# Kernel optimization log

Measured on AMD Instinct MI355X. Metric: run time of the kernel, lower is better.

The kernel has to match this reference:

```python
import jax, jax.numpy as jnp
import numpy as np

K, M_EMB, N_HID, D_CTX, D_ATT, M_COV = 128, 256, 256, 684, 512, 256
B, H, W = 64, 16, 48


def gru_cell(x, h, W_ih, W_hh, b_ih, b_hh):
    # PyTorch GRUCell semantics
    gi = x @ W_ih.T + b_ih
    gh = h @ W_hh.T + b_hh
    i_r, i_z, i_n = jnp.split(gi, 3, axis=-1)
    h_r, h_z, h_n = jnp.split(gh, 3, axis=-1)
    r = jax.nn.sigmoid(i_r + h_r)
    z = jax.nn.sigmoid(i_z + h_z)
    n = jnp.tanh(i_n + r * h_n)
    return (1.0 - z) * n + z * h


def setup_inputs() -> dict:
    key = jax.random.key(0)
    ks = jax.random.split(key, 24)
    s = 0.02
    inp = {
        'y': jax.random.randint(ks[0], (B,), 0, K),
        'y_mask': jnp.ones((B,), jnp.float32),
        'context': jax.random.normal(ks[1], (B, D_CTX, H, W), jnp.float32),
        'pre_hidden': jax.random.normal(ks[2], (B, N_HID), jnp.float32),
        'alpha_past': jax.random.uniform(ks[3], (B, H, W), jnp.float32),
        'emb': jax.random.normal(ks[4], (K + 1, M_EMB)) * s,
        'W_ih1': jax.random.normal(ks[5], (3 * N_HID, M_EMB)) * s,
        'W_hh1': jax.random.normal(ks[6], (3 * N_HID, N_HID)) * s,
        'b_ih1': jnp.zeros((3 * N_HID,)),
        'b_hh1': jnp.zeros((3 * N_HID,)),
        'conv_Ua_w': jax.random.normal(ks[7], (D_ATT, D_CTX, 1, 1)) * s,
        'conv_Ua_b': jnp.zeros((D_ATT,)),
        'Wa': jax.random.normal(ks[8], (D_ATT, N_HID)) * s,
        'conv_Q_w': jax.random.normal(ks[9], (M_COV, 1, 3, 3)) * s,
        'Uf': jax.random.normal(ks[10], (D_ATT, M_COV)) * s,
        'Uf_b': jnp.zeros((D_ATT,)),
        'va': jax.random.normal(ks[11], (1, D_ATT)) * s,
        'va_b': jnp.zeros((1,)),
        'W_ih2': jax.random.normal(ks[12], (3 * N_HID, D_CTX)) * s,
        'W_hh2': jax.random.normal(ks[13], (3 * N_HID, N_HID)) * s,
        'b_ih2': jnp.zeros((3 * N_HID,)),
        'b_hh2': jnp.zeros((3 * N_HID,)),
        'Wct': jax.random.normal(ks[14], (M_EMB, D_CTX)) * s,
        'Wct_b': jnp.zeros((M_EMB,)),
        'Wht': jax.random.normal(ks[15], (M_EMB, N_HID)) * s,
        'Wht_b': jnp.zeros((M_EMB,)),
        'W0': jax.random.normal(ks[16], (K, M_EMB // 2)) * s,
        'W0_b': jnp.zeros((K,)),
    }
    return inp


def reference(y, y_mask, context, pre_hidden, alpha_past, emb,
              W_ih1, W_hh1, b_ih1, b_hh1, conv_Ua_w, conv_Ua_b, Wa,
              conv_Q_w, Uf, Uf_b, va, va_b,
              W_ih2, W_hh2, b_ih2, b_hh2, Wct, Wct_b, Wht, Wht_b, W0, W0_b):
    embedded = emb[y]                                           # [B, m]
    s_hat = gru_cell(embedded, pre_hidden, W_ih1, W_hh1, b_ih1, b_hh1)
    s_hat = y_mask[:, None] * s_hat + (1.0 - y_mask)[:, None] * pre_hidden

    Wa_h1 = s_hat @ Wa.T                                        # [B, A]
    # 1x1 conv == channel projection, output in NHWC layout
    Ua_ctx = jnp.einsum('bdhw,ad->bhwa', context, conv_Ua_w[:, :, 0, 0]) + conv_Ua_b
    # 3x3 coverage conv over past attention map
    cover_F = jax.lax.conv_general_dilated(
        alpha_past[:, None, :, :], conv_Q_w, (1, 1), 'SAME',
        dimension_numbers=('NCHW', 'OIHW', 'NCHW'))              # [B, M, H, W]
    cover_F = jnp.transpose(cover_F, (0, 2, 3, 1))               # [B, H, W, M]
    cover_vector = cover_F @ Uf.T + Uf_b                         # [B, H, W, A]

    e_att = jnp.tanh(Ua_ctx + Wa_h1[:, None, None, :] + cover_vector)
    alpha = (e_att @ va.T + va_b)[..., 0].reshape(e_att.shape[0], -1)  # [B, H*W]
    alpha = jax.nn.softmax(alpha, axis=1)

    ct = jnp.einsum('bdp,bp->bd', context.reshape(context.shape[0], context.shape[1], -1), alpha)

    s = gru_cell(ct, s_hat, W_ih2, W_hh2, b_ih2, b_hh2)
    s = y_mask[:, None] * s + (1.0 - y_mask)[:, None] * s_hat

    logit = ct @ Wct.T + Wct_b + s @ Wht.T + Wht_b + embedded    # [B, m]
    logit = logit.reshape(logit.shape[0], -1, 2).max(axis=2)     # maxout -> [B, m/2]
    out = logit @ W0.T + W0_b                                    # [B, K]
    return out, s, alpha.reshape(alpha.shape[0], H, W)
```

## Files before the change

### kernel.cpp

```cpp
#include <hip/hip_runtime.h>
#include <hip/hip_bf16.h>
#include <math.h>

#define BB 64
#define KV 128
#define ME 256
#define NH 256
#define DC 684
#define DA 512
#define MC 256
#define HH_ 16
#define WW_ 48
#define HW_ 768
#define NS 22

typedef __attribute__((ext_vector_type(8))) short bf16x8;
typedef __attribute__((ext_vector_type(4))) float f32x4;

#define WS_G     0
#define WS_RB    (WS_G + 4608)
#define WS_EMB   (WS_RB + 32768)
#define WS_SH    (WS_EMB + 16384)
#define WS_AL    (WS_SH + 16384)
#define WS_CT    (WS_AL + 49152)
#define WS_APACK (WS_CT + 43776)
#define WS_GI    (WS_APACK + 180224)
#define WS_GH    (WS_GI + 49152)
#define WS_LG    WS_GI
#define WS_BP    (WS_GH + 49152)
#define NEED_BYTES ((size_t)441600 * 4 + (size_t)34603008 * 2)

static __device__ __forceinline__ unsigned short f2b(float v) {
    __hip_bfloat16 h = __float2bfloat16(v);
    return *reinterpret_cast<unsigned short*>(&h);
}

static __device__ __forceinline__ void gl_lds16(const unsigned short* g,
                                                unsigned short* l) {
    __builtin_amdgcn_global_load_lds(
        (const __attribute__((address_space(1))) unsigned int*)g,
        (__attribute__((address_space(3))) unsigned int*)l, 16, 0, 0);
}

__global__ __launch_bounds__(512) void k_prep(
    const float* __restrict__ ctx, const float* __restrict__ Ua,
    const float* __restrict__ Uf, const float* __restrict__ convQ,
    const int* __restrict__ y, const float* __restrict__ emb,
    unsigned short* __restrict__ Bpack, unsigned short* __restrict__ Apack,
    float* __restrict__ G, float* __restrict__ embedded) {
    __shared__ unsigned short Ts[64 * 360];
    int bx = blockIdx.x, t = threadIdx.x;
    if (bx < 768) {
        int b = bx / 12, pt = bx % 12, p0 = pt * 64;
        int w = t >> 6, p = t & 63;
        unsigned short* dst = Bpack + (long)(b * 12 + pt) * 22 * 2048;
        for (int ch = 0; ch < 2; ch++) {
            int dbase = ch * 352;
            if (ch) __syncthreads();
#pragma unroll
            for (int iter = 0; iter < 11; iter++) {
                int d0 = dbase + iter * 32 + w * 4;
                float v0 = 0.f, v1 = 0.f, v2 = 0.f, v3 = 0.f;
                const float* src = ctx + ((long)b * DC + d0) * HW_ + p0 + p;
                if (d0 + 0 < DC) v0 = src[0];
                if (d0 + 1 < DC) v1 = src[HW_];
                if (d0 + 2 < DC) v2 = src[2 * HW_];
                if (d0 + 3 < DC) v3 = src[3 * HW_];
                unsigned u01 = (unsigned)f2b(v0) | ((unsigned)f2b(v1) << 16);
                unsigned u23 = (unsigned)f2b(v2) | ((unsigned)f2b(v3) << 16);
                *(uint2*)&Ts[p * 360 + (d0 - dbase)] = make_uint2(u01, u23);
            }
            __syncthreads();
            int so = t >> 8;
            int tt = t & 255;
            int pp = tt >> 2, slot = tt & 3;
#pragma unroll
            for (int s2 = 0; s2 < 12; s2 += 2) {
                int sl = s2 + so;
                if (sl < 11) {
                    int s = ch * 11 + sl;
                    bf16x8 v = *(const bf16x8*)&Ts[pp * 360 + sl * 32 +
                                                   ((slot ^ ((pp >> 1) & 3))
                                                    << 3)];
                    *(bf16x8*)(dst + (long)(s * 256 + tt) * 8) = v;
                }
            }
        }
    } else if (bx < 856) {
        int bi = bx - 768;
#pragma unroll
        for (int r = 0; r < 8; r++) {
            int idx = bi * 4096 + r * 512 + t;
            int e = idx & 7, slot = (idx >> 3) & 3;
            int a = (idx >> 5) & 511, s = idx >> 14;
            int d = s * 32 + ((slot ^ ((a >> 1) & 3)) << 3) + e;
            float v = (d < DC) ? Ua[a * DC + d] : 0.f;
            Apack[idx] = f2b(v);
        }
    } else if (bx < 865) {
        int idx = (bx - 856) * 512 + t;
        if (idx < DA * 9) {
            int a = idx / 9, k = idx % 9;
            float s = 0.f;
            for (int m = 0; m < MC; m++) s += Uf[a * MC + m] * convQ[m * 9 + k];
            G[idx] = s;
        }
    } else {
        int b = bx - 865;
        if (t < ME) embedded[b * ME + t] = emb[y[b] * ME + t];
    }
}

__global__ __launch_bounds__(256) void k_G(const float* __restrict__ Uf,
                                           const float* __restrict__ convQ,
                                           float* __restrict__ G) {
    int idx = blockIdx.x * 256 + threadIdx.x;
    if (idx >= DA * 9) return;
    int a = idx / 9, k = idx % 9;
    float s = 0.f;
    for (int m = 0; m < MC; m++) s += Uf[a * MC + m] * convQ[m * 9 + k];
    G[idx] = s;
}

__global__ __launch_bounds__(256) void k_prepA(const float* __restrict__ Ua,
                                               unsigned short* __restrict__ Apack) {
    int idx = blockIdx.x * 256 + threadIdx.x;
    if (idx >= NS * DA * 32) return;
    int e = idx & 7, slot = (idx >> 3) & 3;
    int a = (idx >> 5) & 511, s = idx >> 14;
    int d = s * 32 + ((slot ^ ((a >> 1) & 3)) << 3) + e;
    float v = (d < DC) ? Ua[a * DC + d] : 0.f;
    Apack[idx] = f2b(v);
}

__global__ __launch_bounds__(256) void k_emb(const int* __restrict__ y,
                                             const float* __restrict__ emb,
                                             float* __restrict__ embedded) {
    int b = blockIdx.x, t = threadIdx.x;
    embedded[b * ME + t] = emb[y[b] * ME + t];
}

__global__ __launch_bounds__(256) void k_rows256(
    const float* __restrict__ X, const float* __restrict__ W,
    const float* __restrict__ bias, const float* __restrict__ bias2,
    float* __restrict__ out, int outStride) {
    __shared__ float Xs[64 * 257];
    __shared__ float Ws[4 * 260];
    int t = threadIdx.x, w = t >> 6, lane = t & 63;
    for (int i = t; i < 64 * 256; i += 256) {
        int bb = i >> 8, k = i & 255;
        Xs[bb * 257 + k] = X[bb * 256 + k];
    }
    int r = blockIdx.x * 4 + w;
    *(f32x4*)(Ws + w * 260 + lane * 4) = *(const f32x4*)(W + r * 256 + lane * 4);
    __syncthreads();
    const float* xrow = Xs + lane * 257;
    const float* wrow = Ws + w * 260;
    float acc = 0.f;
#pragma unroll 8
    for (int k = 0; k < 256; k++) acc += wrow[k] * xrow[k];
    acc += bias[r];
    if (bias2) acc += bias2[r];
    out[lane * outStride + r] = acc;
}

__global__ __launch_bounds__(256) void k_gih1(
    const float* __restrict__ embedded, const float* __restrict__ pre_hidden,
    const float* __restrict__ W_ih1, const float* __restrict__ W_hh1,
    const float* __restrict__ b_ih1, const float* __restrict__ b_hh1,
    float* __restrict__ gi, float* __restrict__ gh) {
    __shared__ float Xs[64 * 257];
    __shared__ float Ws[4 * 260];
    int bx = blockIdx.x, t = threadIdx.x, w = t >> 6, lane = t & 63;
    const float *X, *W, *bias;
    float* outp;
    int r;
    if (bx < 192) {
        X = embedded; W = W_ih1; bias = b_ih1; outp = gi; r = bx * 4 + w;
    } else {
        X = pre_hidden; W = W_hh1; bias = b_hh1; outp = gh; r = (bx - 192) * 4 + w;
    }
    for (int i = t; i < 64 * 256; i += 256) {
        int bb = i >> 8, k = i & 255;
        Xs[bb * 257 + k] = X[bb * 256 + k];
    }
    *(f32x4*)(Ws + w * 260 + lane * 4) = *(const f32x4*)(W + r * 256 + lane * 4);
    __syncthreads();
    const float* xrow = Xs + lane * 257;
    const float* wrow = Ws + w * 260;
    float acc = 0.f;
#pragma unroll 8
    for (int k = 0; k < 256; k++) acc += wrow[k] * xrow[k];
    outp[lane * 768 + r] = acc + bias[r];
}

__global__ __launch_bounds__(256) void k_gih2(
    const float* __restrict__ ctv, const float* __restrict__ s_hat,
    const float* __restrict__ W_ih2, const float* __restrict__ W_hh2,
    const float* __restrict__ b_ih2, const float* __restrict__ b_hh2,
    float* __restrict__ gi, float* __restrict__ gh) {
    __shared__ float Xs[64 * 257];
    __shared__ float Ws[4 * 260];
    int bx = blockIdx.x, t = threadIdx.x, w = t >> 6, lane = t & 63;
    if (bx < 192) {
        int r = bx * 4 + w;
        float acc = 0.f;
        for (int c = 0; c < 3; c++) {
            int c0 = c * 228;
            __syncthreads();
            for (int i = t; i < 64 * 228; i += 256) {
                int bb = i / 228, kk = i - bb * 228;
                Xs[bb * 229 + kk] = ctv[bb * DC + c0 + kk];
            }
            for (int j = lane; j < 228; j += 64)
                Ws[w * 260 + j] = W_ih2[r * DC + c0 + j];
            __syncthreads();
            const float* xrow = Xs + lane * 229;
            const float* wrow = Ws + w * 260;
#pragma unroll 4
            for (int k = 0; k < 228; k++) acc += wrow[k] * xrow[k];
        }
        gi[lane * 768 + r] = acc + b_ih2[r];
    } else {
        int r = (bx - 192) * 4 + w;
        for (int i = t; i < 64 * 256; i += 256) {
            int bb = i >> 8, k = i & 255;
            Xs[bb * 257 + k] = s_hat[bb * 256 + k];
        }
        *(f32x4*)(Ws + w * 260 + lane * 4) =
            *(const f32x4*)(W_hh2 + r * 256 + lane * 4);
        __syncthreads();
        const float* xrow = Xs + lane * 257;
        const float* wrow = Ws + w * 260;
        float acc = 0.f;
#pragma unroll 8
        for (int k = 0; k < 256; k++) acc += wrow[k] * xrow[k];
        gh[lane * 768 + r] = acc + b_hh2[r];
    }
}

__global__ __launch_bounds__(256) void k_gru(const float* __restrict__ gi,
                                             const float* __restrict__ gh,
                                             const float* __restrict__ h,
                                             const float* __restrict__ y_mask,
                                             float* __restrict__ outp) {
    int b = blockIdx.x, t = threadIdx.x;
    float hv = h[b * NH + t];
    float r = 1.f / (1.f + expf(-(gi[b * 768 + t] + gh[b * 768 + t])));
    float z = 1.f / (1.f + expf(-(gi[b * 768 + 256 + t] + gh[b * 768 + 256 + t])));
    float n = tanhf(gi[b * 768 + 512 + t] + r * gh[b * 768 + 512 + t]);
    float sv = (1.f - z) * n + z * hv;
    float m = y_mask[b];
    outp[b * NH + t] = m * sv + (1.f - m) * hv;
}

__global__ __launch_bounds__(512) void k_att_cnt(
    const unsigned short* __restrict__ Apack,
    const unsigned short* __restrict__ Bpack, const float* __restrict__ G,
    const float* __restrict__ rb, const float* __restrict__ va,
    const float* __restrict__ va_b, const float* __restrict__ apast,
    float* __restrict__ alogit) {
    __shared__ __attribute__((aligned(16))) unsigned short lsA[2][16384];
    __shared__ __attribute__((aligned(16))) unsigned short lsB[2][2048];
    __shared__ float ap_s[18 * 50];
    __shared__ float part_s[8][64];
    int pt = blockIdx.x, b = blockIdx.y;
    int t = threadIdx.x, w = t >> 6, lane = t & 63;
    int l15 = lane & 15, lg = lane >> 4;
    int sx = lg ^ ((l15 >> 1) & 3);

    for (int idx = t; idx < 900; idx += 512) {
        int hh = idx / 50, ww = idx % 50;
        float v = 0.f;
        if (hh >= 1 && hh <= HH_ && ww >= 1 && ww <= WW_)
            v = apast[b * HW_ + (hh - 1) * WW_ + (ww - 1)];
        ap_s[idx] = v;
    }
    __syncthreads();

    const unsigned short* Asrc = Apack + w * 2048 + lane * 8;
    const unsigned short* Bsrc =
        Bpack + (long)(b * 12 + pt) * 22 * 2048 + (w & 3) * 512 + lane * 8;

#define STAGE(S, BUF)                                                        \
    do {                                                                     \
        _Pragma("unroll") for (int i_ = 0; i_ < 4; i_++)                     \
            gl_lds16(Asrc + (long)(S)*16384 + i_ * 512,                      \
                     &lsA[BUF][w * 2048 + i_ * 512]);                        \
        gl_lds16(Bsrc + (long)(S)*2048, &lsB[BUF][(w & 3) * 512]);           \
    } while (0)

#define STEP_BODY(CUR)                                                       \
    do {                                                                     \
        bf16x8 af[4], bf[4];                                                 \
        _Pragma("unroll") for (int j = 0; j < 4; j++)                        \
            bf[j] = *(const bf16x8*)&lsB[CUR][(j * 16 + l15) * 32 + sx * 8]; \
        _Pragma("unroll") for (int i = 0; i < 4; i++)                        \
            af[i] = *(const bf16x8*)&lsA[CUR][(w * 64 + i * 16 + l15) * 32 + \
                                             sx * 8];                        \
        _Pragma("unroll") for (int i = 0; i < 4; i++)                        \
            _Pragma("unroll") for (int j = 0; j < 4; j++)                    \
                acc[i][j] = __builtin_amdgcn_mfma_f32_16x16x32_bf16(         \
                    af[i], bf[j], acc[i][j], 0, 0, 0);                       \
    } while (0)

    f32x4 acc[4][4];
#pragma unroll
    for (int i = 0; i < 4; i++)
#pragma unroll
        for (int j = 0; j < 4; j++) acc[i][j] = {0.f, 0.f, 0.f, 0.f};

    STAGE(0, 0);
    STAGE(1, 1);

    for (int s = 0; s < NS - 1; s++) {
        int cur = s & 1;
        asm volatile("s_waitcnt vmcnt(5)" ::: "memory");
        __builtin_amdgcn_sched_barrier(0);
        __builtin_amdgcn_s_barrier();
        __builtin_amdgcn_sched_barrier(0);
        STEP_BODY(cur);
        __builtin_amdgcn_s_barrier();
        __builtin_amdgcn_sched_barrier(0);
        if (s + 2 < NS) STAGE(s + 2, cur);
    }
    asm volatile("s_waitcnt vmcnt(0)" ::: "memory");
    __builtin_amdgcn_sched_barrier(0);
    __builtin_amdgcn_s_barrier();
    __builtin_amdgcn_sched_barrier(0);
    STEP_BODY((NS - 1) & 1);
#undef STAGE
#undef STEP_BODY

    float partial[4] = {0.f, 0.f, 0.f, 0.f};
#pragma unroll
    for (int i = 0; i < 4; i++) {
#pragma unroll
        for (int r = 0; r < 4; r++) {
            int a = w * 64 + i * 16 + lg * 4 + r;
            float rbv = rb[b * DA + a];
            float vav = va[a];
            const float* Ga = G + a * 9;
            float g0 = Ga[0], g1 = Ga[1], g2 = Ga[2], g3 = Ga[3], g4 = Ga[4];
            float g5 = Ga[5], g6 = Ga[6], g7 = Ga[7], g8 = Ga[8];
#pragma unroll
            for (int j = 0; j < 4; j++) {
                int p = pt * 64 + j * 16 + l15;
                int hh = p / WW_, ww = p % WW_;
                const float* ap = ap_s + hh * 50 + ww;
                float cov = g0 * ap[0] + g1 * ap[1] + g2 * ap[2] +
                            g3 * ap[50] + g4 * ap[51] + g5 * ap[52] +
                            g6 * ap[100] + g7 * ap[101] + g8 * ap[102];
                float e = tanhf(acc[i][j][r] + rbv + cov);
                partial[j] += vav * e;
            }
        }
    }
#pragma unroll
    for (int j = 0; j < 4; j++) {
        partial[j] += __shfl_xor(partial[j], 16);
        partial[j] += __shfl_xor(partial[j], 32);
    }
    if (lane < 16) {
#pragma unroll
        for (int j = 0; j < 4; j++) part_s[w][j * 16 + lane] = partial[j];
    }
    __syncthreads();
    if (t < 64) {
        float sum = va_b[0];
#pragma unroll
        for (int q = 0; q < 8; q++) sum += part_s[q][t];
        alogit[b * HW_ + pt * 64 + t] = sum;
    }
}

#define LDW 40
__global__ __launch_bounds__(256) void k_att_lds(
    const unsigned short* __restrict__ Apack, const float* __restrict__ ctx,
    const float* __restrict__ G, const float* __restrict__ rb,
    const float* __restrict__ va, const float* __restrict__ va_b,
    const float* __restrict__ apast, float* __restrict__ alogit) {
    __shared__ __attribute__((aligned(16))) short lsB[2][64 * LDW];
    __shared__ float ap_s[18 * 50];
    __shared__ float part_s[4 * 64];
    int b = blockIdx.y;
    int p0 = blockIdx.x * 64;
    int t = threadIdx.x;
    int w = t >> 6, lane = t & 63;
    int l15 = lane & 15, lg = lane >> 4;
    int sxA = lg ^ ((l15 >> 1) & 3);
    int pq = t & 15, kp = t >> 4;
    const float* ctx_b = ctx + (long)b * DC * HW_ + p0;

    for (int idx = t; idx < 900; idx += 256) {
        int hh = idx / 50, ww = idx % 50;
        float v = 0.f;
        if (hh >= 1 && hh <= HH_ && ww >= 1 && ww <= WW_)
            v = apast[b * HW_ + (hh - 1) * WW_ + (ww - 1)];
        ap_s[idx] = v;
    }

#define CTXLOAD(FA, FB, S)                                                   \
    do {                                                                     \
        int d_ = (S) * 32 + 2 * kp;                                          \
        const float* s0_ = ctx_b + (long)d_ * HW_ + pq;                      \
        bool g0_ = d_ < DC, g1_ = (d_ + 1) < DC;                             \
        _Pragma("unroll") for (int j_ = 0; j_ < 4; j_++) {                   \
            FA[j_] = g0_ ? s0_[16 * j_] : 0.f;                               \
            FB[j_] = g1_ ? s0_[HW_ + 16 * j_] : 0.f;                         \
        }                                                                    \
    } while (0)
#define STAGEW(FA, FB, BUF)                                                  \
    do {                                                                     \
        _Pragma("unroll") for (int j_ = 0; j_ < 4; j_++) {                   \
            ((unsigned*)lsB[BUF])[(pq + 16 * j_) * (LDW / 2) + kp] =         \
                (unsigned)f2b(FA[j_]) | ((unsigned)f2b(FB[j_]) << 16);       \
        }                                                                    \
    } while (0)
#define ALOAD(AF, S)                                                         \
    do {                                                                     \
        _Pragma("unroll") for (int i_ = 0; i_ < 8; i_++)                     \
            AF[i_] = *(const bf16x8*)(Apack +                                \
                ((long)((S)*512 + w * 128 + i_ * 16 + l15) * 4 + sxA) * 8);  \
    } while (0)
#define BREAD(BF, BUF)                                                       \
    do {                                                                     \
        _Pragma("unroll") for (int j_ = 0; j_ < 4; j_++)                     \
            BF[j_] = *(const bf16x8*)(&lsB[BUF][(j_ * 16 + l15) * LDW +      \
                                               lg * 8]);                     \
    } while (0)
#define MFMA8x4(AF, BF)                                                      \
    do {                                                                     \
        _Pragma("unroll") for (int i_ = 0; i_ < 8; i_++)                     \
            _Pragma("unroll") for (int j_ = 0; j_ < 4; j_++)                 \
                acc[i_][j_] = __builtin_amdgcn_mfma_f32_16x16x32_bf16(       \
                    AF[i_], BF[j_], acc[i_][j_], 0, 0, 0);                   \
    } while (0)

    f32x4 acc[8][4];
#pragma unroll
    for (int i = 0; i < 8; i++)
#pragma unroll
        for (int j = 0; j < 4; j++) acc[i][j] = {0.f, 0.f, 0.f, 0.f};

    float fa0[4], fb0[4], fa1[4], fb1[4];
    bf16x8 afr0[8], afr1[8], bfr[4];

    CTXLOAD(fa1, fb1, 0);
    ALOAD(afr0, 0);
    STAGEW(fa1, fb1, 0);
    CTXLOAD(fa1, fb1, 1);
    __syncthreads();

    for (int ss = 0; ss < NS; ss += 2) {
        if (ss + 2 < NS) CTXLOAD(fa0, fb0, ss + 2);
        ALOAD(afr1, ss + 1);
        BREAD(bfr, 0);
        STAGEW(fa1, fb1, 1);
        MFMA8x4(afr0, bfr);
        __syncthreads();
        if (ss + 3 < NS) CTXLOAD(fa1, fb1, ss + 3);
        if (ss + 2 < NS) {
            ALOAD(afr0, ss + 2);
            BREAD(bfr, 1);
            STAGEW(fa0, fb0, 0);
            MFMA8x4(afr1, bfr);
        } else {
            BREAD(bfr, 1);
            MFMA8x4(afr1, bfr);
        }
        __syncthreads();
    }

    float partial[4] = {0.f, 0.f, 0.f, 0.f};
#pragma unroll
    for (int i = 0; i < 8; i++) {
#pragma unroll
        for (int r = 0; r < 4; r++) {
            int a = w * 128 + i * 16 + lg * 4 + r;
            float rbv = rb[b * DA + a];
            float vav = va[a];
            const float* Ga = G + a * 9;
            float g0 = Ga[0], g1 = Ga[1], g2 = Ga[2], g3 = Ga[3], g4 = Ga[4];
            float g5 = Ga[5], g6 = Ga[6], g7 = Ga[7], g8 = Ga[8];
#pragma unroll
            for (int j = 0; j < 4; j++) {
                int p = p0 + j * 16 + l15;
                int hh = p / WW_, ww = p % WW_;
                const float* ap = ap_s + hh * 50 + ww;
                float cov = g0 * ap[0] + g1 * ap[1] + g2 * ap[2] +
                            g3 * ap[50] + g4 * ap[51] + g5 * ap[52] +
                            g6 * ap[100] + g7 * ap[101] + g8 * ap[102];
                float e = tanhf(acc[i][j][r] + rbv + cov);
                partial[j] += vav * e;
            }
        }
    }
#pragma unroll
    for (int j = 0; j < 4; j++) {
        partial[j] += __shfl_xor(partial[j], 16);
        partial[j] += __shfl_xor(partial[j], 32);
    }
    if (lane < 16) {
#pragma unroll
        for (int j = 0; j < 4; j++) part_s[w * 64 + j * 16 + lane] = partial[j];
    }
    __syncthreads();
    if (t < 64) {
        float s = va_b[0] + part_s[t] + part_s[64 + t] + part_s[128 + t] +
                  part_s[192 + t];
        alogit[b * HW_ + p0 + t] = s;
    }
}

__global__ __launch_bounds__(256) void k_ctsm(const float* __restrict__ ctx,
                                              const float* __restrict__ alogit,
                                              float* __restrict__ ct,
                                              float* __restrict__ alpha_out) {
    __shared__ float al_s[HW_];
    __shared__ float red[16];
    int b = blockIdx.y, t = threadIdx.x;
    float v[3];
    float mx = -1e30f;
    for (int i = 0; i < 3; i++) {
        v[i] = alogit[b * HW_ + i * 256 + t];
        mx = fmaxf(mx, v[i]);
    }
    for (int off = 32; off > 0; off >>= 1) mx = fmaxf(mx, __shfl_down(mx, off));
    if ((t & 63) == 0) red[t >> 6] = mx;
    __syncthreads();
    if (t == 0) red[0] = fmaxf(fmaxf(red[0], red[1]), fmaxf(red[2], red[3]));
    __syncthreads();
    mx = red[0];
    float sum = 0.f;
    for (int i = 0; i < 3; i++) {
        v[i] = expf(v[i] - mx);
        sum += v[i];
    }
    for (int off = 32; off > 0; off >>= 1) sum += __shfl_down(sum, off);
    if ((t & 63) == 0) red[8 + (t >> 6)] = sum;
    __syncthreads();
    if (t == 0) red[8] = red[8] + red[9] + red[10] + red[11];
    __syncthreads();
    float inv = 1.f / red[8];
    for (int i = 0; i < 3; i++) {
        float a = v[i] * inv;
        al_s[i * 256 + t] = a;
        if (blockIdx.x == 0) alpha_out[b * HW_ + i * 256 + t] = a;
    }
    __syncthreads();
    int dc0 = blockIdx.x * 114;
    int wave = t >> 6, lane = t & 63;
    for (int d = dc0 + wave; d < dc0 + 114; d += 4) {
        const float* row = &ctx[((long)b * DC + d) * HW_];
        float s = 0.f;
#pragma unroll
        for (int q = 0; q < 12; q++) s += row[lane + q * 64] * al_s[lane + q * 64];
        for (int off = 32; off > 0; off >>= 1) s += __shfl_down(s, off);
        if (lane == 0) ct[b * DC + d] = s;
    }
}

__global__ __launch_bounds__(256) void k_logit(
    const float* __restrict__ ctv, const float* __restrict__ s,
    const float* __restrict__ embedded, const float* __restrict__ Wct,
    const float* __restrict__ Wht, const float* __restrict__ Wct_b,
    const float* __restrict__ Wht_b, float* __restrict__ lg) {
    __shared__ float Xs[64 * 257];
    __shared__ float Ws[4 * 232];
    int t = threadIdx.x, w = t >> 6, lane = t & 63;
    int r = blockIdx.x * 4 + w;
    float acc = 0.f;
    for (int c = 0; c < 3; c++) {
        int c0 = c * 228;
        __syncthreads();
        for (int i = t; i < 64 * 228; i += 256) {
            int bb = i / 228, kk = i - bb * 228;
            Xs[bb * 229 + kk] = ctv[bb * DC + c0 + kk];
        }
        for (int j = lane; j < 228; j += 64) Ws[w * 232 + j] = Wct[r * DC + c0 + j];
        __syncthreads();
        const float* xrow = Xs + lane * 229;
        const float* wrow = Ws + w * 232;
#pragma unroll 4
        for (int k = 0; k < 228; k++) acc += wrow[k] * xrow[k];
    }
    __syncthreads();
    for (int i = t; i < 64 * 256; i += 256) {
        int bb = i >> 8, k = i & 255;
        Xs[bb * 257 + k] = s[bb * 256 + k];
    }
    __syncthreads();
    const float* xrow2 = Xs + lane * 257;
    const float* wr = Wht + r * 256;
    float acc2 = 0.f;
#pragma unroll 8
    for (int k = 0; k < 256; k++) acc2 += wr[k] * xrow2[k];
    lg[lane * 256 + r] = acc + acc2 + Wct_b[r] + Wht_b[r] + embedded[lane * 256 + r];
}

__global__ __launch_bounds__(256) void k_head(const float* __restrict__ lg,
                                              const float* __restrict__ W0,
                                              const float* __restrict__ W0_b,
                                              float* __restrict__ out) {
    __shared__ float Xs[64 * 129];
    __shared__ float Ws[4 * 132];
    int t = threadIdx.x, w = t >> 6, lane = t & 63;
    for (int i = t; i < 64 * 128; i += 256) {
        int bb = i >> 7, m = i & 127;
        Xs[bb * 129 + m] = fmaxf(lg[bb * 256 + 2 * m], lg[bb * 256 + 2 * m + 1]);
    }
    int r = blockIdx.x * 4 + w;
    Ws[w * 132 + lane] = W0[r * 128 + lane];
    Ws[w * 132 + 64 + lane] = W0[r * 128 + 64 + lane];
    __syncthreads();
    const float* xrow = Xs + lane * 129;
    const float* wrow = Ws + w * 132;
    float acc = 0.f;
#pragma unroll 8
    for (int k = 0; k < 128; k++) acc += wrow[k] * xrow[k];
    out[lane * KV + r] = acc + W0_b[r];
}

extern "C" void kernel_launch(void* const* d_in, const int* in_sizes, int n_in,
                              void* d_out, int out_size, void* d_ws,
                              size_t ws_size, hipStream_t stream) {
    const int* y = (const int*)d_in[0];
    const float* y_mask = (const float*)d_in[1];
    const float* context = (const float*)d_in[2];
    const float* pre_hidden = (const float*)d_in[3];
    const float* alpha_past = (const float*)d_in[4];
    const float* emb = (const float*)d_in[5];
    const float* W_ih1 = (const float*)d_in[6];
    const float* W_hh1 = (const float*)d_in[7];
    const float* b_ih1 = (const float*)d_in[8];
    const float* b_hh1 = (const float*)d_in[9];
    const float* conv_Ua_w = (const float*)d_in[10];
    const float* conv_Ua_b = (const float*)d_in[11];
    const float* Wa = (const float*)d_in[12];
    const float* conv_Q_w = (const float*)d_in[13];
    const float* Uf = (const float*)d_in[14];
    const float* Uf_b = (const float*)d_in[15];
    const float* va = (const float*)d_in[16];
    const float* va_b = (const float*)d_in[17];
    const float* W_ih2 = (const float*)d_in[18];
    const float* W_hh2 = (const float*)d_in[19];
    const float* b_ih2 = (const float*)d_in[20];
    const float* b_hh2 = (const float*)d_in[21];
    const float* Wct = (const float*)d_in[22];
    const float* Wct_b = (const float*)d_in[23];
    const float* Wht = (const float*)d_in[24];
    const float* Wht_b = (const float*)d_in[25];
    const float* W0 = (const float*)d_in[26];
    const float* W0_b = (const float*)d_in[27];

    float* ws = (float*)d_ws;
    float* out = (float*)d_out;
    float* G = ws + WS_G;
    float* rbias = ws + WS_RB;
    float* embedded = ws + WS_EMB;
    float* s_hat = ws + WS_SH;
    float* alogit = ws + WS_AL;
    float* ctv = ws + WS_CT;
    unsigned short* Apack = (unsigned short*)(ws + WS_APACK);
    float* gi = ws + WS_GI;
    float* gh = ws + WS_GH;
    float* lg = ws + WS_LG;
    unsigned short* Bpack = (unsigned short*)(ws + WS_BP);
    float* s_out = out + 8192;
    float* alpha_out = out + 24576;

    bool fast = ws_size >= NEED_BYTES;

    if (fast) {
        k_prep<<<dim3(929), dim3(512), 0, stream>>>(context, conv_Ua_w, Uf,
                                                    conv_Q_w, y, emb, Bpack,
                                                    Apack, G, embedded);
    } else {
        k_G<<<dim3(18), dim3(256), 0, stream>>>(Uf, conv_Q_w, G);
        k_prepA<<<dim3((NS * DA * 32 + 255) / 256), dim3(256), 0, stream>>>(
            conv_Ua_w, Apack);
        k_emb<<<dim3(64), dim3(256), 0, stream>>>(y, emb, embedded);
    }
    k_gih1<<<dim3(384), dim3(256), 0, stream>>>(embedded, pre_hidden, W_ih1,
                                                W_hh1, b_ih1, b_hh1, gi, gh);
    k_gru<<<dim3(64), dim3(256), 0, stream>>>(gi, gh, pre_hidden, y_mask, s_hat);
    k_rows256<<<dim3(128), dim3(256), 0, stream>>>(s_hat, Wa, conv_Ua_b, Uf_b,
                                                   rbias, 512);
    if (fast) {
        k_att_cnt<<<dim3(12, 64), dim3(512), 0, stream>>>(
            Apack, Bpack, G, rbias, va, va_b, alpha_past, alogit);
    } else {
        k_att_lds<<<dim3(12, 64), dim3(256), 0, stream>>>(
            Apack, context, G, rbias, va, va_b, alpha_past, alogit);
    }
    k_ctsm<<<dim3(6, 64), dim3(256), 0, stream>>>(context, alogit, ctv,
                                                  alpha_out);
    k_gih2<<<dim3(384), dim3(256), 0, stream>>>(ctv, s_hat, W_ih2, W_hh2, b_ih2,
                                                b_hh2, gi, gh);
    k_gru<<<dim3(64), dim3(256), 0, stream>>>(gi, gh, s_hat, y_mask, s_out);
    k_logit<<<dim3(64), dim3(256), 0, stream>>>(ctv, s_out, embedded, Wct, Wht,
                                                Wct_b, Wht_b, lg);
    k_head<<<dim3(32), dim3(256), 0, stream>>>(lg, W0, W0_b, out);
}
```

Before: 247.7 us.

## Split attention GEMM across two attention-dim halves with partial logits

The fused attention-score kernel now launches twice as many 256-thread blocks, each covering half of the 512 attention dimensions. Each block writes a partial logit, and the softmax/context kernel adds the two halves when it reads them. The aim is more parallelism and occupancy through smaller LDS and thread counts per block. The cost is that each context B tile is loaded twice and extra workspace is needed. The va_b bias is dropped because softmax is invariant to adding a constant.

```diff
diff --git a/kernel.cpp b/kernel.cpp
--- a/kernel.cpp
+++ b/kernel.cpp
@@ -28,7 +28,8 @@
 #define WS_GH    (WS_GI + 49152)
 #define WS_LG    WS_GI
 #define WS_BP    (WS_GH + 49152)
-#define NEED_BYTES ((size_t)441600 * 4 + (size_t)34603008 * 2)
+#define WS_ALQ   (WS_BP + 17301504)
+#define NEED_BYTES ((size_t)(441600 + 17301504 + 98304) * 4)
 
 static __device__ __forceinline__ unsigned short f2b(float v) {
     __hip_bfloat16 h = __float2bfloat16(v);
@@ -254,22 +255,21 @@
     outp[b * NH + t] = m * sv + (1.f - m) * hv;
 }
 
-__global__ __launch_bounds__(512) void k_att_cnt(
+__global__ __launch_bounds__(256) void k_att3(
     const unsigned short* __restrict__ Apack,
     const unsigned short* __restrict__ Bpack, const float* __restrict__ G,
     const float* __restrict__ rb, const float* __restrict__ va,
-    const float* __restrict__ va_b, const float* __restrict__ apast,
-    float* __restrict__ alogit) {
-    __shared__ __attribute__((aligned(16))) unsigned short lsA[2][16384];
+    const float* __restrict__ apast, float* __restrict__ alq) {
+    __shared__ __attribute__((aligned(16))) unsigned short lsA[2][8192];
     __shared__ __attribute__((aligned(16))) unsigned short lsB[2][2048];
     __shared__ float ap_s[18 * 50];
-    __shared__ float part_s[8][64];
-    int pt = blockIdx.x, b = blockIdx.y;
+    __shared__ float part_s[4][64];
+    int pt = blockIdx.x, ah = blockIdx.y, b = blockIdx.z;
     int t = threadIdx.x, w = t >> 6, lane = t & 63;
     int l15 = lane & 15, lg = lane >> 4;
     int sx = lg ^ ((l15 >> 1) & 3);
 
-    for (int idx = t; idx < 900; idx += 512) {
+    for (int idx = t; idx < 900; idx += 256) {
         int hh = idx / 50, ww = idx % 50;
         float v = 0.f;
         if (hh >= 1 && hh <= HH_ && ww >= 1 && ww <= WW_)
@@ -278,26 +278,26 @@
     }
     __syncthreads();
 
-    const unsigned short* Asrc = Apack + w * 2048 + lane * 8;
-    const unsigned short* Bsrc =
-        Bpack + (long)(b * 12 + pt) * 22 * 2048 + (w & 3) * 512 + lane * 8;
+    const unsigned short* Ap0 = Apack + ah * 8192 + w * 2048 + lane * 8;
+    const unsigned short* Bp0 =
+        Bpack + (long)(b * 12 + pt) * 22 * 2048 + w * 512 + lane * 8;
 
 #define STAGE(S, BUF)                                                        \
     do {                                                                     \
         _Pragma("unroll") for (int i_ = 0; i_ < 4; i_++)                     \
-            gl_lds16(Asrc + (long)(S)*16384 + i_ * 512,                      \
+            gl_lds16(Ap0 + (long)(S)*16384 + i_ * 512,                       \
                      &lsA[BUF][w * 2048 + i_ * 512]);                        \
-        gl_lds16(Bsrc + (long)(S)*2048, &lsB[BUF][(w & 3) * 512]);           \
+        gl_lds16(Bp0 + (long)(S)*2048, &lsB[BUF][w * 512]);                  \
     } while (0)
 
 #define STEP_BODY(CUR)                                                       \
     do {                                                                     \
         bf16x8 af[4], bf[4];                                                 \
-        _Pragma("unroll") for (int j = 0; j < 4; j++)                        \
-            bf[j] = *(const bf16x8*)&lsB[CUR][(j * 16 + l15) * 32 + sx * 8]; \
         _Pragma("unroll") for (int i = 0; i < 4; i++)                        \
             af[i] = *(const bf16x8*)&lsA[CUR][(w * 64 + i * 16 + l15) * 32 + \
                                              sx * 8];                        \
+        _Pragma("unroll") for (int j = 0; j < 4; j++)                        \
+            bf[j] = *(const bf16x8*)&lsB[CUR][(j * 16 + l15) * 32 + sx * 8]; \
         _Pragma("unroll") for (int i = 0; i < 4; i++)                        \
             _Pragma("unroll") for (int j = 0; j < 4; j++)                    \
                 acc[i][j] = __builtin_amdgcn_mfma_f32_16x16x32_bf16(         \
@@ -337,7 +337,7 @@
     for (int i = 0; i < 4; i++) {
 #pragma unroll
         for (int r = 0; r < 4; r++) {
-            int a = w * 64 + i * 16 + lg * 4 + r;
+            int a = ah * 256 + w * 64 + i * 16 + lg * 4 + r;
             float rbv = rb[b * DA + a];
             float vav = va[a];
             const float* Ga = G + a * 9;
@@ -367,10 +367,9 @@
     }
     __syncthreads();
     if (t < 64) {
-        float sum = va_b[0];
-#pragma unroll
-        for (int q = 0; q < 8; q++) sum += part_s[q][t];
-        alogit[b * HW_ + pt * 64 + t] = sum;
+        float sum = (part_s[0][t] + part_s[1][t]) +
+                    (part_s[2][t] + part_s[3][t]);
+        alq[ah * 49152 + b * HW_ + pt * 64 + t] = sum;
     }
 }
 
@@ -378,8 +377,8 @@
 __global__ __launch_bounds__(256) void k_att_lds(
     const unsigned short* __restrict__ Apack, const float* __restrict__ ctx,
     const float* __restrict__ G, const float* __restrict__ rb,
-    const float* __restrict__ va, const float* __restrict__ va_b,
-    const float* __restrict__ apast, float* __restrict__ alogit) {
+    const float* __restrict__ va, const float* __restrict__ apast,
+    float* __restrict__ alogit) {
     __shared__ __attribute__((aligned(16))) short lsB[2][64 * LDW];
     __shared__ float ap_s[18 * 50];
     __shared__ float part_s[4 * 64];
@@ -507,14 +506,14 @@
     }
     __syncthreads();
     if (t < 64) {
-        float s = va_b[0] + part_s[t] + part_s[64 + t] + part_s[128 + t] +
+        float s = part_s[t] + part_s[64 + t] + part_s[128 + t] +
                   part_s[192 + t];
         alogit[b * HW_ + p0 + t] = s;
     }
 }
 
 __global__ __launch_bounds__(256) void k_ctsm(const float* __restrict__ ctx,
-                                              const float* __restrict__ alogit,
+                                              const float* __restrict__ alq,
                                               float* __restrict__ ct,
                                               float* __restrict__ alpha_out) {
     __shared__ float al_s[HW_];
@@ -523,7 +522,8 @@
     float v[3];
     float mx = -1e30f;
     for (int i = 0; i < 3; i++) {
-        v[i] = alogit[b * HW_ + i * 256 + t];
+        int idx = b * HW_ + i * 256 + t;
+        v[i] = alq[idx] + alq[49152 + idx];
         mx = fmaxf(mx, v[i]);
     }
     for (int off = 32; off > 0; off >>= 1) mx = fmaxf(mx, __shfl_down(mx, off));
@@ -660,13 +660,13 @@
     float* rbias = ws + WS_RB;
     float* embedded = ws + WS_EMB;
     float* s_hat = ws + WS_SH;
-    float* alogit = ws + WS_AL;
     float* ctv = ws + WS_CT;
     unsigned short* Apack = (unsigned short*)(ws + WS_APACK);
     float* gi = ws + WS_GI;
     float* gh = ws + WS_GH;
     float* lg = ws + WS_LG;
     unsigned short* Bpack = (unsigned short*)(ws + WS_BP);
+    float* alq = ws + WS_ALQ;
     float* s_out = out + 8192;
     float* alpha_out = out + 24576;
 
@@ -688,14 +688,14 @@
     k_rows256<<<dim3(128), dim3(256), 0, stream>>>(s_hat, Wa, conv_Ua_b, Uf_b,
                                                    rbias, 512);
     if (fast) {
-        k_att_cnt<<<dim3(12, 64), dim3(512), 0, stream>>>(
-            Apack, Bpack, G, rbias, va, va_b, alpha_past, alogit);
+        k_att3<<<dim3(12, 2, 64), dim3(256), 0, stream>>>(
+            Apack, Bpack, G, rbias, va, alpha_past, alq);
     } else {
+        hipMemsetAsync(alq + 49152, 0, (size_t)49152 * sizeof(float), stream);
         k_att_lds<<<dim3(12, 64), dim3(256), 0, stream>>>(
-            Apack, context, G, rbias, va, va_b, alpha_past, alogit);
-    }
-    k_ctsm<<<dim3(6, 64), dim3(256), 0, stream>>>(context, alogit, ctv,
-                                                  alpha_out);
+            Apack, context, G, rbias, va, alpha_past, alq);
+    }
+    k_ctsm<<<dim3(6, 64), dim3(256), 0, stream>>>(context, alq, ctv, alpha_out);
     k_gih2<<<dim3(384), dim3(256), 0, stream>>>(ctv, s_hat, W_ih2, W_hh2, b_ih2,
                                                 b_hh2, gi, gh);
     k_gru<<<dim3(64), dim3(256), 0, stream>>>(gi, gh, s_hat, y_mask, s_out);
```

Result: slower. 299.9 us (+21.1%).
